# Optimization experiments

Hardware: AMD Instinct MI355X
Metric: run time of the kernel (lower is better)

The kernel has to match this reference:

```python
import jax, jax.numpy as jnp
import numpy as np

B, N, DIM, H, DH = 2, 4096, 512, 8, 64  # inner_dim = H*DH = 512


def setup_inputs() -> dict:
    key = jax.random.key(0)
    ks = jax.random.split(key, 4)
    x = jax.random.normal(ks[0], (B, N, DIM), dtype=jnp.float32)
    Wq = jax.random.normal(ks[1], (DIM, H * DH), dtype=jnp.float32) * (DIM ** -0.5)
    Wkv = jax.random.normal(ks[2], (DIM, 2 * H * DH), dtype=jnp.float32) * (DIM ** -0.5)
    Wo = jax.random.normal(ks[3], (H * DH, DIM), dtype=jnp.float32) * ((H * DH) ** -0.5)
    bo = jnp.zeros((DIM,), dtype=jnp.float32)
    return {"x": x, "Wq": Wq, "Wkv": Wkv, "Wo": Wo, "bo": bo}


def reference(x, Wq, Wkv, Wo, bo):
    scale = DH ** -0.5
    # projections (context defaults to x -> self-attention)
    q = x @ Wq
    kv = x @ Wkv
    k, v = jnp.split(kv, 2, axis=-1)
    # NOTE: original code scales q by dim_head**-0.5 in forward() AND again
    # inside attention(), i.e. an effective dim_head**-1 scaling. Faithful.
    q = q * scale
    # b n (h d) -> b h n d
    split_heads = lambda t: t.reshape(B, N, H, DH).transpose(0, 2, 1, 3)
    q, k, v = map(split_heads, (q, k, v))
    q = q * scale  # second scaling inside attention()
    sim = jnp.einsum('bhid,bhjd->bhij', q, k)  # [B,H,N,N] full score matrix
    sim = sim - jax.lax.stop_gradient(jnp.max(sim, axis=-1, keepdims=True))
    mask_value = -jnp.finfo(sim.dtype).max
    causal_mask = jnp.triu(jnp.ones((N, N), dtype=bool), k=1)
    sim = jnp.where(causal_mask, mask_value, sim)
    attn = jax.nn.softmax(sim, axis=-1)
    out = jnp.einsum('bhij,bhjd->bhid', attn, v)
    out = out.transpose(0, 2, 1, 3).reshape(B, N, H * DH)  # b h n d -> b n (h d)
    return out @ Wo + bo
```

## Files before the change

kernel.cpp:

```cpp
#include <hip/hip_runtime.h>

typedef short s16x8 __attribute__((ext_vector_type(8)));
typedef short s16x4 __attribute__((ext_vector_type(4)));
typedef float f32x4 __attribute__((ext_vector_type(4)));
typedef unsigned short u16;
typedef unsigned int u32;

#define MFMA16(a, b, c) __builtin_amdgcn_mfma_f32_16x16x32_bf16((a), (b), (c), 0, 0, 0)
#define MFMA1616(a, b, c) __builtin_amdgcn_mfma_f32_16x16x16bf16_1k((a), (b), (c), 0, 0, 0)

__device__ __forceinline__ u16 f2bf(float f) {
  u32 u = __float_as_uint(f);
  u += 0x7fffu + ((u >> 16) & 1u);
  return (u16)(u >> 16);
}
__device__ __forceinline__ u16 f2bf_fast(float f) {
  return (u16)((__float_as_uint(f) + 0x8000u) >> 16);
}
__device__ __forceinline__ float bf2f(u16 u) {
  return __uint_as_float(((u32)u) << 16);
}
__device__ __forceinline__ float ex2(float x) {
  float r;
  asm("v_exp_f32 %0, %1" : "=v"(r) : "v"(x));
  return r;
}
__device__ __forceinline__ void gll(const u16* g, u16* l) {
  __builtin_amdgcn_global_load_lds((const __attribute__((address_space(1))) u32*)g,
                                   (__attribute__((address_space(3))) u32*)l, 16, 0, 0);
}

__global__ __launch_bounds__(256) void k_prep(const float* __restrict__ x,
                                              const float* __restrict__ Wq,
                                              const float* __restrict__ Wkv,
                                              const float* __restrict__ Wo,
                                              u16* __restrict__ xb,
                                              u16* __restrict__ wqkvt,
                                              u16* __restrict__ wot) {
  const int bx = blockIdx.x, t = threadIdx.x;
  if (bx < 4096) {
    int i = bx * 256 + t;
    float4 v = ((const float4*)x)[i];
    ushort4 o;
    o.x = f2bf(v.x); o.y = f2bf(v.y); o.z = f2bf(v.z); o.w = f2bf(v.w);
    ((ushort4*)xb)[i] = o;
    return;
  }
  __shared__ u16 tl[64 * 66];
  const float* src; u16* dst; int N, kb, nb;
  if (bx < 4160)      { int tb = bx - 4096; src = Wq;  dst = wqkvt;          N = 512;  kb = tb >> 3; nb = tb & 7; }
  else if (bx < 4288) { int tb = bx - 4160; src = Wkv; dst = wqkvt + 262144; N = 1024; kb = tb >> 4; nb = tb & 15; }
  else                { int tb = bx - 4288; src = Wo;  dst = wot;            N = 512;  kb = tb >> 3; nb = tb & 7; }
#pragma unroll
  for (int it = 0; it < 4; ++it) {
    int idx = it * 256 + t;
    int kl = idx >> 4, nc = idx & 15;
    float4 v = *(const float4*)(src + (kb * 64 + kl) * N + nb * 64 + nc * 4);
    u16* p = &tl[kl * 66 + nc * 4];
    p[0] = f2bf(v.x); p[1] = f2bf(v.y); p[2] = f2bf(v.z); p[3] = f2bf(v.w);
  }
  __syncthreads();
#pragma unroll
  for (int it = 0; it < 2; ++it) {
    int idx = it * 256 + t;
    int nl = idx >> 3, kc = idx & 7;
    u16 tmp[8];
#pragma unroll
    for (int j = 0; j < 8; ++j) tmp[j] = tl[(kc * 8 + j) * 66 + nl];
    *(s16x8*)(dst + (nb * 64 + nl) * 512 + kb * 64 + kc * 8) = *(const s16x8*)tmp;
  }
}

__global__ __launch_bounds__(256, 2) void k_gemm_qkv(
    const u16* __restrict__ A, const u16* __restrict__ Bt,
    u16* __restrict__ Qb, u16* __restrict__ Kb, u16* __restrict__ Vg) {
  __shared__ __align__(16) u16 As[8192], Bs[8192];
  const int t = threadIdx.x, w = t >> 6, l = t & 63, quad = l >> 4, lr = l & 15;
  const int bm = blockIdx.x, bn = blockIdx.y;
  const int wm = (w >> 1) * 64, wn = (w & 1) * 64;
  const f32x4 fz = {0.f, 0.f, 0.f, 0.f};
  f32x4 acc[4][4];
#pragma unroll
  for (int i = 0; i < 4; ++i)
#pragma unroll
    for (int j = 0; j < 4; ++j) acc[i][j] = fz;
  const u16* Ag = A + bm * 128 * 512;
  const u16* Bg = Bt + bn * 128 * 512;
  for (int kk = 0; kk < 8; ++kk) {
    __syncthreads();
#pragma unroll
    for (int i = 0; i < 4; ++i) {
      int ci = w * 256 + i * 64 + l;
      int row = ci >> 3, cb = ci & 7;
      int off = row * 512 + kk * 64 + ((cb ^ (row & 7)) << 3);
      gll(Ag + off, &As[w * 2048 + i * 512]);
      gll(Bg + off, &Bs[w * 2048 + i * 512]);
    }
    __syncthreads();
    s16x8 af[4][2], bf[4][2];
#pragma unroll
    for (int x2 = 0; x2 < 4; ++x2)
#pragma unroll
      for (int c = 0; c < 2; ++c) {
        int sw = ((c * 4 + quad) ^ (lr & 7)) << 3;
        af[x2][c] = *(const s16x8*)&As[(wm + x2 * 16 + lr) * 64 + sw];
        bf[x2][c] = *(const s16x8*)&Bs[(wn + x2 * 16 + lr) * 64 + sw];
      }
#pragma unroll
    for (int c = 0; c < 2; ++c)
#pragma unroll
      for (int ti = 0; ti < 4; ++ti)
#pragma unroll
        for (int tj = 0; tj < 4; ++tj)
          acc[ti][tj] = MFMA16(af[ti][c], bf[tj][c], acc[ti][tj]);
  }
  const int buf = (bn * 128) >> 9;
  const float QS = 0.0225421107f;
#pragma unroll
  for (int ti = 0; ti < 4; ++ti)
#pragma unroll
    for (int tj = 0; tj < 4; ++tj) {
      int col = bn * 128 + wn + tj * 16 + lr;
      int hd = col & 511, h = hd >> 6, d = hd & 63;
      int row0 = bm * 128 + wm + ti * 16 + quad * 4;
      int b = row0 >> 12, n0 = row0 & 4095;
      long base = (long)(b * 8 + h) * 262144;
      if (buf == 0) {
#pragma unroll
        for (int r = 0; r < 4; ++r) Qb[base + (long)(n0 + r) * 64 + d] = f2bf(acc[ti][tj][r] * QS);
      } else if (buf == 1) {
#pragma unroll
        for (int r = 0; r < 4; ++r) Kb[base + (long)(n0 + r) * 64 + d] = f2bf(acc[ti][tj][r]);
      } else {
        ushort4 pk;
        pk.x = f2bf(acc[ti][tj][0]); pk.y = f2bf(acc[ti][tj][1]);
        pk.z = f2bf(acc[ti][tj][2]); pk.w = f2bf(acc[ti][tj][3]);
        long vaddr = base + ((long)((n0 >> 6) * 4 + ((n0 >> 4) & 3)) * 4 + (d >> 4)) * 256
                     + (long)(d & 15) * 16 + (n0 & 15);
        *(ushort4*)&Vg[vaddr] = pk;
      }
    }
}

__global__ __launch_bounds__(256, 2) void k_gemm_out(
    const u16* __restrict__ A, const u16* __restrict__ Bt,
    const float* __restrict__ bias, float* __restrict__ out) {
  __shared__ __align__(16) u16 As[8192], Bs[8192];
  const int t = threadIdx.x, w = t >> 6, l = t & 63, quad = l >> 4, lr = l & 15;
  const int bm = blockIdx.x, bn = blockIdx.y;
  const int wm = (w >> 1) * 64, wn = (w & 1) * 64;
  const f32x4 fz = {0.f, 0.f, 0.f, 0.f};
  f32x4 acc[4][4];
#pragma unroll
  for (int i = 0; i < 4; ++i)
#pragma unroll
    for (int j = 0; j < 4; ++j) acc[i][j] = fz;
  const u16* Ag = A + bm * 128 * 512;
  const u16* Bg = Bt + bn * 128 * 512;
  for (int kk = 0; kk < 8; ++kk) {
    __syncthreads();
#pragma unroll
    for (int i = 0; i < 4; ++i) {
      int ci = w * 256 + i * 64 + l;
      int row = ci >> 3, cb = ci & 7;
      int off = row * 512 + kk * 64 + ((cb ^ (row & 7)) << 3);
      gll(Ag + off, &As[w * 2048 + i * 512]);
      gll(Bg + off, &Bs[w * 2048 + i * 512]);
    }
    __syncthreads();
    s16x8 af[4][2], bf[4][2];
#pragma unroll
    for (int x2 = 0; x2 < 4; ++x2)
#pragma unroll
      for (int c = 0; c < 2; ++c) {
        int sw = ((c * 4 + quad) ^ (lr & 7)) << 3;
        af[x2][c] = *(const s16x8*)&As[(wm + x2 * 16 + lr) * 64 + sw];
        bf[x2][c] = *(const s16x8*)&Bs[(wn + x2 * 16 + lr) * 64 + sw];
      }
#pragma unroll
    for (int c = 0; c < 2; ++c)
#pragma unroll
      for (int ti = 0; ti < 4; ++ti)
#pragma unroll
        for (int tj = 0; tj < 4; ++tj)
          acc[ti][tj] = MFMA16(af[ti][c], bf[tj][c], acc[ti][tj]);
  }
#pragma unroll
  for (int ti = 0; ti < 4; ++ti)
#pragma unroll
    for (int tj = 0; tj < 4; ++tj) {
      int col = bn * 128 + wn + tj * 16 + lr;
      float bb = bias[col];
#pragma unroll
      for (int r = 0; r < 4; ++r) {
        int row = bm * 128 + wm + ti * 16 + quad * 4 + r;
        out[(long)row * 512 + col] = acc[ti][tj][r] + bb;
      }
    }
}

__global__ __launch_bounds__(128, 2) void k_attn_split(
    const u16* __restrict__ Qb, const u16* __restrict__ Kb,
    const u16* __restrict__ Vg, u16* __restrict__ pO,
    float* __restrict__ pM, float* __restrict__ pL) {
  const int bid = blockIdx.x;
  const int qt = 63 - (bid >> 6), rem = bid & 63, bh = rem >> 2, c = rem & 3;
  const int jcount = qt + 1;
  const int nc = (jcount + 15) >> 4;
  if (c >= nc) return;
  const int jstart = c * 16;
  const int jendx = (jstart + 16 < jcount) ? jstart + 16 : jcount;
  __shared__ __align__(16) u16 lds[4096];
  const int t = threadIdx.x, w = t >> 6, l = t & 63, quad = l >> 4, lr = l & 15;
  const u16* Qh = Qb + (long)bh * 262144;
  const u16* Kh = Kb + (long)bh * 262144;
  const u16* Vh = Vg + (long)bh * 262144;
  const int rw0 = qt * 64 + w * 32;
  s16x8 qf[2][2];
#pragma unroll
  for (int mt = 0; mt < 2; ++mt)
#pragma unroll
    for (int cc = 0; cc < 2; ++cc)
      qf[mt][cc] = *(const s16x8*)(Qh + (rw0 + mt * 16 + lr) * 64 + cc * 32 + quad * 8);
  const f32x4 fz = {0.f, 0.f, 0.f, 0.f};
  f32x4 o[2][4];
#pragma unroll
  for (int mt = 0; mt < 2; ++mt)
#pragma unroll
    for (int dt = 0; dt < 4; ++dt) o[mt][dt] = fz;
  float m_r[2] = {-3.0e38f, -3.0e38f};
  float lp[2] = {0.f, 0.f};
  const int voff = lr * 16 + quad * 4;

  for (int jt = jstart; jt < jendx; ++jt) {
    __syncthreads();
    const u16* Ksrc = Kh + jt * 4096;
#pragma unroll
    for (int i = 0; i < 4; ++i) {
      int ci = (w * 4 + i) * 64 + l;
      int row = ci >> 3, cb = ci & 7;
      int sw = (cb ^ (row & 7)) << 3;
      gll(Ksrc + row * 64 + sw, &lds[(w * 4 + i) * 512]);
    }
    const u16* Vsrc = Vh + jt * 4096 + voff;
    s16x4 av[4][4];
#pragma unroll
    for (int nt = 0; nt < 4; ++nt)
#pragma unroll
      for (int dt = 0; dt < 4; ++dt)
        av[nt][dt] = *(const s16x4*)(Vsrc + (nt * 4 + dt) * 256);
    __syncthreads();
    if (jt * 64 >= rw0 + 32) continue;
    f32x4 s[2][4];
#pragma unroll
    for (int mt = 0; mt < 2; ++mt)
#pragma unroll
      for (int nt = 0; nt < 4; ++nt) s[mt][nt] = fz;
#pragma unroll
    for (int cc = 0; cc < 2; ++cc) {
      s16x8 kbf[4];
#pragma unroll
      for (int nt = 0; nt < 4; ++nt)
        kbf[nt] = *(const s16x8*)&lds[(nt * 16 + lr) * 64 + (((cc * 4 + quad) ^ (lr & 7)) << 3)];
#pragma unroll
      for (int mt = 0; mt < 2; ++mt)
#pragma unroll
        for (int nt = 0; nt < 4; ++nt)
          s[mt][nt] = MFMA16(kbf[nt], qf[mt][cc], s[mt][nt]);
    }
    const bool dg = (jt * 64 + 63 > rw0);
    s16x4 pf[2][4];
#pragma unroll
    for (int mt = 0; mt < 2; ++mt) {
      if (dg) {
        int T = rw0 + mt * 16 + lr - jt * 64;
#pragma unroll
        for (int nt = 0; nt < 4; ++nt)
#pragma unroll
          for (int r = 0; r < 4; ++r)
            if (nt * 16 + quad * 4 + r > T) s[mt][nt][r] = -1e30f;
      }
      float lm = fmaxf(fmaxf(fmaxf(s[mt][0][0], s[mt][0][1]), fmaxf(s[mt][0][2], s[mt][0][3])),
                       fmaxf(fmaxf(s[mt][1][0], s[mt][1][1]), fmaxf(s[mt][1][2], s[mt][1][3])));
      float lm2 = fmaxf(fmaxf(fmaxf(s[mt][2][0], s[mt][2][1]), fmaxf(s[mt][2][2], s[mt][2][3])),
                        fmaxf(fmaxf(s[mt][3][0], s[mt][3][1]), fmaxf(s[mt][3][2], s[mt][3][3])));
      lm = fmaxf(lm, lm2);
      lm = fmaxf(lm, __shfl_xor(lm, 16));
      lm = fmaxf(lm, __shfl_xor(lm, 32));
      float mn = fmaxf(m_r[mt], lm);
      float al = ex2(m_r[mt] - mn);
      m_r[mt] = mn;
      float ts = 0.f;
#pragma unroll
      for (int nt = 0; nt < 4; ++nt)
#pragma unroll
        for (int r = 0; r < 4; ++r) {
          float p = ex2(s[mt][nt][r] - mn);
          s[mt][nt][r] = p;
          ts += p;
        }
      lp[mt] = lp[mt] * al + ts;
#pragma unroll
      for (int nt = 0; nt < 4; ++nt) {
        s16x4 pk;
        pk[0] = (short)f2bf_fast(s[mt][nt][0]);
        pk[1] = (short)f2bf_fast(s[mt][nt][1]);
        pk[2] = (short)f2bf_fast(s[mt][nt][2]);
        pk[3] = (short)f2bf_fast(s[mt][nt][3]);
        pf[mt][nt] = pk;
      }
#pragma unroll
      for (int dt = 0; dt < 4; ++dt)
#pragma unroll
        for (int r = 0; r < 4; ++r) o[mt][dt][r] *= al;
    }
#pragma unroll
    for (int nt = 0; nt < 4; ++nt)
#pragma unroll
      for (int mt = 0; mt < 2; ++mt)
#pragma unroll
        for (int dt = 0; dt < 4; ++dt)
          o[mt][dt] = MFMA1616(av[nt][dt], pf[mt][nt], o[mt][dt]);
  }
  const int pidx = (bh * 64 + qt) * 4 + c;
#pragma unroll
  for (int mt = 0; mt < 2; ++mt) {
    float lv = lp[mt];
    lv += __shfl_xor(lv, 16);
    lv += __shfl_xor(lv, 32);
    if (quad == 0) {
      pM[pidx * 64 + w * 32 + mt * 16 + lr] = m_r[mt];
      pL[pidx * 64 + w * 32 + mt * 16 + lr] = lv;
    }
#pragma unroll
    for (int dt = 0; dt < 4; ++dt) {
      ushort4 pk;
      pk.x = f2bf(o[mt][dt][0]); pk.y = f2bf(o[mt][dt][1]);
      pk.z = f2bf(o[mt][dt][2]); pk.w = f2bf(o[mt][dt][3]);
      *(ushort4*)&pO[(long)pidx * 4096 + (w * 32 + mt * 16 + lr) * 64 + dt * 16 + quad * 4] = pk;
    }
  }
}

__global__ __launch_bounds__(128) void k_comb(const u16* __restrict__ pO,
                                              const float* __restrict__ pM,
                                              const float* __restrict__ pL,
                                              u16* __restrict__ Ob) {
  const int bid = blockIdx.x, t = threadIdx.x;
  const int bh = bid >> 6, qt = bid & 63;
  const int nc = (qt + 16) >> 4;
  const int row = t >> 1, half = t & 1;
  const int pbase = (bh * 64 + qt) * 4;
  float M = -3.0e38f;
  for (int c = 0; c < nc; ++c) M = fmaxf(M, pM[(pbase + c) * 64 + row]);
  float L = 0.f;
  float acc[32];
#pragma unroll
  for (int d = 0; d < 32; ++d) acc[d] = 0.f;
  for (int c = 0; c < nc; ++c) {
    float wgt = ex2(pM[(pbase + c) * 64 + row] - M);
    L += pL[(pbase + c) * 64 + row] * wgt;
    const u16* src = pO + (long)(pbase + c) * 4096 + row * 64 + half * 32;
#pragma unroll
    for (int k = 0; k < 4; ++k) {
      s16x8 v = *(const s16x8*)(src + k * 8);
#pragma unroll
      for (int j = 0; j < 8; ++j) acc[k * 8 + j] += wgt * bf2f((u16)v[j]);
    }
  }
  float inv = 1.0f / L;
  u16 tmp[32];
#pragma unroll
  for (int d = 0; d < 32; ++d) tmp[d] = f2bf(acc[d] * inv);
  const int b = bh >> 3, h = bh & 7;
  long gbase = (long)(b * 4096 + qt * 64 + row) * 512 + h * 64 + half * 32;
#pragma unroll
  for (int k = 0; k < 4; ++k)
    *(s16x8*)(Ob + gbase + k * 8) = *(const s16x8*)(tmp + k * 8);
}

extern "C" void kernel_launch(void* const* d_in, const int* in_sizes, int n_in,
                              void* d_out, int out_size, void* d_ws, size_t ws_size,
                              hipStream_t stream) {
  const float* x   = (const float*)d_in[0];
  const float* Wq  = (const float*)d_in[1];
  const float* Wkv = (const float*)d_in[2];
  const float* Wo  = (const float*)d_in[3];
  const float* bo  = (const float*)d_in[4];
  float* out = (float*)d_out;
  char* ws = (char*)d_ws;
  const size_t MB = 1048576;
  u16* wot   = (u16*)(ws);
  u16* wqkvt = (u16*)(ws + MB / 2);
  u16* Qb    = (u16*)(ws + 2 * MB);
  u16* Kb    = (u16*)(ws + 10 * MB);
  u16* Vg    = (u16*)(ws + 18 * MB);
  u16* Ob    = (u16*)(ws + 26 * MB);
  u16* xbf   = (u16*)(ws + 34 * MB);
  u16* pO    = (u16*)(ws + 34 * MB);
  float* pM  = (float*)(ws + 66 * MB);
  float* pL  = (float*)(ws + 67 * MB);

  k_prep<<<4352, 256, 0, stream>>>(x, Wq, Wkv, Wo, xbf, wqkvt, wot);
  k_gemm_qkv<<<dim3(64, 12), 256, 0, stream>>>(xbf, wqkvt, Qb, Kb, Vg);
  k_attn_split<<<4096, 128, 0, stream>>>(Qb, Kb, Vg, pO, pM, pL);
  k_comb<<<1024, 128, 0, stream>>>(pO, pM, pL, Ob);
  k_gemm_out<<<dim3(64, 4), 256, 0, stream>>>(Ob, wot, bo, out);
}
```

Baseline: 229.2 us.

## Double-buffer K tiles in LDS and V fragments in registers for prefetch

Restructures the split attention loop so that the K tile for the next iteration goes into a second LDS buffer and the matching V fragments go into a second register set while the current tile is computed. The goal is to hide global load latency behind the MFMA and softmax work, and to cut the two barriers per tile down to one. The cost is a doubled LDS footprint, extra VGPRs for the second V register set, and loss of the early skip for a wave whose rows lie fully above the diagonal tile, so that wave now does fully masked work.

```diff
diff --git a/kernel.cpp b/kernel.cpp
--- a/kernel.cpp
+++ b/kernel.cpp
@@ -199,6 +199,102 @@
     }
 }
 
+__device__ __forceinline__ void stage_tile(const u16* Kh, const u16* Vh, int jt,
+                                           u16* ldsbuf, s16x4 (&av)[4][4],
+                                           int w, int l, int voff) {
+  const u16* Ksrc = Kh + jt * 4096;
+#pragma unroll
+  for (int i = 0; i < 4; ++i) {
+    int ci = (w * 4 + i) * 64 + l;
+    int row = ci >> 3, cb = ci & 7;
+    int sw = (cb ^ (row & 7)) << 3;
+    gll(Ksrc + row * 64 + sw, ldsbuf + (w * 4 + i) * 512);
+  }
+  const u16* Vsrc = Vh + jt * 4096 + voff;
+#pragma unroll
+  for (int nt = 0; nt < 4; ++nt)
+#pragma unroll
+    for (int dt = 0; dt < 4; ++dt)
+      av[nt][dt] = *(const s16x4*)(Vsrc + (nt * 4 + dt) * 256);
+}
+
+__device__ __forceinline__ void attn_tile(const u16* Ks, const s16x4 (&av)[4][4],
+                                          const s16x8 (&qf)[2][2], f32x4 (&o)[2][4],
+                                          float (&m_r)[2], float (&lp)[2],
+                                          int jt, int rw0, int quad, int lr) {
+  const f32x4 fz = {0.f, 0.f, 0.f, 0.f};
+  f32x4 s[2][4];
+#pragma unroll
+  for (int mt = 0; mt < 2; ++mt)
+#pragma unroll
+    for (int nt = 0; nt < 4; ++nt) s[mt][nt] = fz;
+#pragma unroll
+  for (int cc = 0; cc < 2; ++cc) {
+    s16x8 kbf[4];
+#pragma unroll
+    for (int nt = 0; nt < 4; ++nt)
+      kbf[nt] = *(const s16x8*)&Ks[(nt * 16 + lr) * 64 + (((cc * 4 + quad) ^ (lr & 7)) << 3)];
+#pragma unroll
+    for (int mt = 0; mt < 2; ++mt)
+#pragma unroll
+      for (int nt = 0; nt < 4; ++nt)
+        s[mt][nt] = MFMA16(kbf[nt], qf[mt][cc], s[mt][nt]);
+  }
+  const bool dg = (jt * 64 + 63 > rw0);
+  s16x4 pf[2][4];
+#pragma unroll
+  for (int mt = 0; mt < 2; ++mt) {
+    if (dg) {
+      int T = rw0 + mt * 16 + lr - jt * 64;
+#pragma unroll
+      for (int nt = 0; nt < 4; ++nt)
+#pragma unroll
+        for (int r = 0; r < 4; ++r)
+          if (nt * 16 + quad * 4 + r > T) s[mt][nt][r] = -1e30f;
+    }
+    float lm = fmaxf(fmaxf(fmaxf(s[mt][0][0], s[mt][0][1]), fmaxf(s[mt][0][2], s[mt][0][3])),
+                     fmaxf(fmaxf(s[mt][1][0], s[mt][1][1]), fmaxf(s[mt][1][2], s[mt][1][3])));
+    float lm2 = fmaxf(fmaxf(fmaxf(s[mt][2][0], s[mt][2][1]), fmaxf(s[mt][2][2], s[mt][2][3])),
+                      fmaxf(fmaxf(s[mt][3][0], s[mt][3][1]), fmaxf(s[mt][3][2], s[mt][3][3])));
+    lm = fmaxf(lm, lm2);
+    lm = fmaxf(lm, __shfl_xor(lm, 16));
+    lm = fmaxf(lm, __shfl_xor(lm, 32));
+    float mn = fmaxf(m_r[mt], lm);
+    float al = ex2(m_r[mt] - mn);
+    m_r[mt] = mn;
+    float ts = 0.f;
+#pragma unroll
+    for (int nt = 0; nt < 4; ++nt)
+#pragma unroll
+      for (int r = 0; r < 4; ++r) {
+        float p = ex2(s[mt][nt][r] - mn);
+        s[mt][nt][r] = p;
+        ts += p;
+      }
+    lp[mt] = lp[mt] * al + ts;
+#pragma unroll
+    for (int nt = 0; nt < 4; ++nt) {
+      s16x4 pk;
+      pk[0] = (short)f2bf_fast(s[mt][nt][0]);
+      pk[1] = (short)f2bf_fast(s[mt][nt][1]);
+      pk[2] = (short)f2bf_fast(s[mt][nt][2]);
+      pk[3] = (short)f2bf_fast(s[mt][nt][3]);
+      pf[mt][nt] = pk;
+    }
+#pragma unroll
+    for (int dt = 0; dt < 4; ++dt)
+#pragma unroll
+      for (int r = 0; r < 4; ++r) o[mt][dt][r] *= al;
+  }
+#pragma unroll
+  for (int nt = 0; nt < 4; ++nt)
+#pragma unroll
+    for (int mt = 0; mt < 2; ++mt)
+#pragma unroll
+      for (int dt = 0; dt < 4; ++dt)
+        o[mt][dt] = MFMA1616(av[nt][dt], pf[mt][nt], o[mt][dt]);
+}
+
 __global__ __launch_bounds__(128, 2) void k_attn_split(
     const u16* __restrict__ Qb, const u16* __restrict__ Kb,
     const u16* __restrict__ Vg, u16* __restrict__ pO,
@@ -210,12 +306,15 @@
   if (c >= nc) return;
   const int jstart = c * 16;
   const int jendx = (jstart + 16 < jcount) ? jstart + 16 : jcount;
-  __shared__ __align__(16) u16 lds[4096];
+  __shared__ __align__(16) u16 lds[8192];
   const int t = threadIdx.x, w = t >> 6, l = t & 63, quad = l >> 4, lr = l & 15;
   const u16* Qh = Qb + (long)bh * 262144;
   const u16* Kh = Kb + (long)bh * 262144;
   const u16* Vh = Vg + (long)bh * 262144;
   const int rw0 = qt * 64 + w * 32;
+  const int voff = lr * 16 + quad * 4;
+  s16x4 av0[4][4], av1[4][4];
+  stage_tile(Kh, Vh, jstart, &lds[0], av0, w, l, voff);
   s16x8 qf[2][2];
 #pragma unroll
   for (int mt = 0; mt < 2; ++mt)
@@ -230,97 +329,20 @@
     for (int dt = 0; dt < 4; ++dt) o[mt][dt] = fz;
   float m_r[2] = {-3.0e38f, -3.0e38f};
   float lp[2] = {0.f, 0.f};
-  const int voff = lr * 16 + quad * 4;
-
-  for (int jt = jstart; jt < jendx; ++jt) {
-    __syncthreads();
-    const u16* Ksrc = Kh + jt * 4096;
-#pragma unroll
-    for (int i = 0; i < 4; ++i) {
-      int ci = (w * 4 + i) * 64 + l;
-      int row = ci >> 3, cb = ci & 7;
-      int sw = (cb ^ (row & 7)) << 3;
-      gll(Ksrc + row * 64 + sw, &lds[(w * 4 + i) * 512]);
-    }
-    const u16* Vsrc = Vh + jt * 4096 + voff;
-    s16x4 av[4][4];
-#pragma unroll
-    for (int nt = 0; nt < 4; ++nt)
-#pragma unroll
-      for (int dt = 0; dt < 4; ++dt)
-        av[nt][dt] = *(const s16x4*)(Vsrc + (nt * 4 + dt) * 256);
-    __syncthreads();
-    if (jt * 64 >= rw0 + 32) continue;
-    f32x4 s[2][4];
-#pragma unroll
-    for (int mt = 0; mt < 2; ++mt)
-#pragma unroll
-      for (int nt = 0; nt < 4; ++nt) s[mt][nt] = fz;
-#pragma unroll
-    for (int cc = 0; cc < 2; ++cc) {
-      s16x8 kbf[4];
-#pragma unroll
-      for (int nt = 0; nt < 4; ++nt)
-        kbf[nt] = *(const s16x8*)&lds[(nt * 16 + lr) * 64 + (((cc * 4 + quad) ^ (lr & 7)) << 3)];
-#pragma unroll
-      for (int mt = 0; mt < 2; ++mt)
-#pragma unroll
-        for (int nt = 0; nt < 4; ++nt)
-          s[mt][nt] = MFMA16(kbf[nt], qf[mt][cc], s[mt][nt]);
-    }
-    const bool dg = (jt * 64 + 63 > rw0);
-    s16x4 pf[2][4];
-#pragma unroll
-    for (int mt = 0; mt < 2; ++mt) {
-      if (dg) {
-        int T = rw0 + mt * 16 + lr - jt * 64;
-#pragma unroll
-        for (int nt = 0; nt < 4; ++nt)
-#pragma unroll
-          for (int r = 0; r < 4; ++r)
-            if (nt * 16 + quad * 4 + r > T) s[mt][nt][r] = -1e30f;
-      }
-      float lm = fmaxf(fmaxf(fmaxf(s[mt][0][0], s[mt][0][1]), fmaxf(s[mt][0][2], s[mt][0][3])),
-                       fmaxf(fmaxf(s[mt][1][0], s[mt][1][1]), fmaxf(s[mt][1][2], s[mt][1][3])));
-      float lm2 = fmaxf(fmaxf(fmaxf(s[mt][2][0], s[mt][2][1]), fmaxf(s[mt][2][2], s[mt][2][3])),
-                        fmaxf(fmaxf(s[mt][3][0], s[mt][3][1]), fmaxf(s[mt][3][2], s[mt][3][3])));
-      lm = fmaxf(lm, lm2);
-      lm = fmaxf(lm, __shfl_xor(lm, 16));
-      lm = fmaxf(lm, __shfl_xor(lm, 32));
-      float mn = fmaxf(m_r[mt], lm);
-      float al = ex2(m_r[mt] - mn);
-      m_r[mt] = mn;
-      float ts = 0.f;
-#pragma unroll
-      for (int nt = 0; nt < 4; ++nt)
-#pragma unroll
-        for (int r = 0; r < 4; ++r) {
-          float p = ex2(s[mt][nt][r] - mn);
-          s[mt][nt][r] = p;
-          ts += p;
-        }
-      lp[mt] = lp[mt] * al + ts;
-#pragma unroll
-      for (int nt = 0; nt < 4; ++nt) {
-        s16x4 pk;
-        pk[0] = (short)f2bf_fast(s[mt][nt][0]);
-        pk[1] = (short)f2bf_fast(s[mt][nt][1]);
-        pk[2] = (short)f2bf_fast(s[mt][nt][2]);
-        pk[3] = (short)f2bf_fast(s[mt][nt][3]);
-        pf[mt][nt] = pk;
-      }
-#pragma unroll
-      for (int dt = 0; dt < 4; ++dt)
-#pragma unroll
-        for (int r = 0; r < 4; ++r) o[mt][dt][r] *= al;
-    }
-#pragma unroll
-    for (int nt = 0; nt < 4; ++nt)
-#pragma unroll
-      for (int mt = 0; mt < 2; ++mt)
-#pragma unroll
-        for (int dt = 0; dt < 4; ++dt)
-          o[mt][dt] = MFMA1616(av[nt][dt], pf[mt][nt], o[mt][dt]);
+  __syncthreads();
+
+  int jt = jstart;
+  while (true) {
+    if (jt + 1 < jendx) stage_tile(Kh, Vh, jt + 1, &lds[4096], av1, w, l, voff);
+    attn_tile(&lds[0], av0, qf, o, m_r, lp, jt, rw0, quad, lr);
+    __syncthreads();
+    ++jt;
+    if (jt >= jendx) break;
+    if (jt + 1 < jendx) stage_tile(Kh, Vh, jt + 1, &lds[0], av0, w, l, voff);
+    attn_tile(&lds[4096], av1, qf, o, m_r, lp, jt, rw0, quad, lr);
+    __syncthreads();
+    ++jt;
+    if (jt >= jendx) break;
   }
   const int pidx = (bh * 64 + qt) * 4 + c;
 #pragma unroll
```

Result: faster. 216.0 us (-5.7%).
